# Optimization experiments

Hardware: AMD Instinct MI355X
Metric: run time of the kernel (lower is better)

The kernel has to match this reference:

```python
import jax, jax.numpy as jnp
import numpy as np

N, D, C = 4096, 2048, 8192
NUM_IDS = 256
MARGIN = 0.3
LABEL_SMOOTHING = 0.1


def setup_inputs() -> dict:
    key = jax.random.key(0)
    k1, k2, k3 = jax.random.split(key, 3)
    embeddings = jax.random.normal(k1, (N, D), dtype=jnp.float32)
    pred_ids = jax.random.normal(k2, (N, C), dtype=jnp.float32)
    target_ids = jax.random.randint(k3, (N,), 0, NUM_IDS, dtype=jnp.int64)
    return {"embeddings": embeddings, "pred_ids": pred_ids, "target_ids": target_ids}


def _euclidean_dist(x, y):
    xx = jnp.sum(x * x, axis=1, keepdims=True)            # [N,1]
    yy = jnp.sum(y * y, axis=1, keepdims=True).T          # [1,N]
    d2 = xx + yy - 2.0 * (x @ y.T)
    return jnp.sqrt(jnp.maximum(d2, 1e-12))


def _cross_entropy_ls(logits, targets, eps):
    # label-smoothed CE, mean over batch
    logp = jax.nn.log_softmax(logits, axis=-1)
    n_cls = logits.shape[-1]
    nll = -jnp.take_along_axis(logp, targets[:, None], axis=1)[:, 0]
    smooth = -jnp.mean(logp, axis=-1)
    return jnp.mean((1.0 - eps) * nll + eps * smooth)


def reference(embeddings, pred_ids, target_ids):
    # ID loss: cross entropy with label smoothing
    id_loss = _cross_entropy_ls(pred_ids, target_ids, LABEL_SMOOTHING)

    # Triplet loss with batch-hard mining
    dist = _euclidean_dist(embeddings, embeddings)        # [N,N]
    pos_mask = target_ids[:, None] == target_ids[None, :] # includes diagonal (as in original)
    neg_inf = jnp.float32(-jnp.inf)
    pos_inf = jnp.float32(jnp.inf)
    dist_ap = jnp.max(jnp.where(pos_mask, dist, neg_inf), axis=1)  # hardest positive
    dist_an = jnp.min(jnp.where(pos_mask, pos_inf, dist), axis=1)  # hardest negative

    # MarginRankingLoss with y=1: mean(relu(dist_ap - dist_an + margin))
    tri_loss = jnp.mean(jnp.maximum(dist_ap - dist_an + MARGIN, 0.0))

    return (id_loss, tri_loss, dist_ap, dist_an)
```

## Files before the change

### kernel.cpp

```cpp
#include <hip/hip_runtime.h>
#include <hip/hip_bf16.h>

typedef unsigned short u16;
typedef unsigned int u32;
typedef __attribute__((ext_vector_type(8))) __bf16 bf16x8;
typedef __attribute__((ext_vector_type(4))) float f32x4;

#define NROW 4096
#define DDIM 2048
#define NCLS 8192
#define MARGIN 0.3f
#define EPS_LS 0.1f
#define FLT_MAX_ 3.402823466e+38f

#define GLOBAL_AS __attribute__((address_space(1)))
#define LDS_AS __attribute__((address_space(3)))

__device__ __forceinline__ void gload_lds16(const void* g, void* l) {
    __builtin_amdgcn_global_load_lds((const GLOBAL_AS u32*)g, (LDS_AS u32*)l, 16, 0, 0);
}

__device__ __forceinline__ u16 f2bf(float f) {
    u32 b = __float_as_uint(f);
    u32 r = (b + 0x7FFFu + ((b >> 16) & 1u)) >> 16;
    return (u16)r;
}

__global__ __launch_bounds__(256) void prep_kernel(
    const float* __restrict__ emb, u16* __restrict__ e16,
    float* __restrict__ xx, int* __restrict__ ap, int* __restrict__ an)
{
    int row = blockIdx.x, tid = threadIdx.x;
    const float4* p = (const float4*)(emb + (size_t)row * DDIM);
    float4 a = p[tid * 2], b = p[tid * 2 + 1];
    float s = a.x*a.x + a.y*a.y + a.z*a.z + a.w*a.w
            + b.x*b.x + b.y*b.y + b.z*b.z + b.w*b.w;

    uint4 pk;
    pk.x = (u32)f2bf(a.x) | ((u32)f2bf(a.y) << 16);
    pk.y = (u32)f2bf(a.z) | ((u32)f2bf(a.w) << 16);
    pk.z = (u32)f2bf(b.x) | ((u32)f2bf(b.y) << 16);
    pk.w = (u32)f2bf(b.z) | ((u32)f2bf(b.w) << 16);
    *(uint4*)&e16[(size_t)row * DDIM + tid * 8] = pk;

    #pragma unroll
    for (int o = 1; o < 64; o <<= 1) s += __shfl_xor(s, o);
    __shared__ float sred[4];
    if ((tid & 63) == 0) sred[tid >> 6] = s;
    __syncthreads();
    if (tid == 0) {
        xx[row] = sred[0] + sred[1] + sred[2] + sred[3];
        ap[row] = 0x80000000;
        an[row] = 0x7FFFFFFF;
    }
}

__device__ __forceinline__ void ce_block(
    int row, const float* __restrict__ pred, const int* __restrict__ tgt,
    float* __restrict__ out, float* smem )
{
    int tid = threadIdx.x;
    const float4* p = (const float4*)(pred + (size_t)row * NCLS);
    float4 v[8];
    #pragma unroll
    for (int i = 0; i < 8; ++i) v[i] = p[tid + i * 256];

    float mx = -FLT_MAX_, sm = 0.f;
    #pragma unroll
    for (int i = 0; i < 8; ++i) {
        mx = fmaxf(mx, fmaxf(fmaxf(v[i].x, v[i].y), fmaxf(v[i].z, v[i].w)));
        sm += v[i].x + v[i].y + v[i].z + v[i].w;
    }
    #pragma unroll
    for (int o = 1; o < 64; o <<= 1) {
        mx = fmaxf(mx, __shfl_xor(mx, o));
        sm += __shfl_xor(sm, o);
    }
    float* smx = smem; float* ssm = smem + 4; float* sse = smem + 8;
    int w = tid >> 6;
    if ((tid & 63) == 0) { smx[w] = mx; ssm[w] = sm; }
    __syncthreads();
    mx = fmaxf(fmaxf(smx[0], smx[1]), fmaxf(smx[2], smx[3]));
    sm = ssm[0] + ssm[1] + ssm[2] + ssm[3];

    float es = 0.f;
    #pragma unroll
    for (int i = 0; i < 8; ++i) {
        es += expf(v[i].x - mx) + expf(v[i].y - mx)
            + expf(v[i].z - mx) + expf(v[i].w - mx);
    }
    #pragma unroll
    for (int o = 1; o < 64; o <<= 1) es += __shfl_xor(es, o);
    if ((tid & 63) == 0) sse[w] = es;
    __syncthreads();
    if (tid == 0) {
        es = sse[0] + sse[1] + sse[2] + sse[3];
        float lse = mx + logf(es);
        int t = tgt[row];
        float lt = pred[(size_t)row * NCLS + t];
        float loss = (1.0f - EPS_LS) * (lse - lt)
                   + EPS_LS * (lse - sm * (1.0f / NCLS));
        atomicAdd(out, loss * (1.0f / NROW));
    }
}

__global__ __launch_bounds__(256) void fused_kernel(
    const u16* __restrict__ e16, const float* __restrict__ xx,
    const int* __restrict__ tg, int* __restrict__ ap, int* __restrict__ an,
    const float* __restrict__ pred, float* __restrict__ out)
{
    __shared__ __align__(16) u16 lsA[64 * 64];
    __shared__ __align__(16) u16 lsB[128 * 64];
    __shared__ float cered[12];

    int bid = blockIdx.x;
    int q = bid / 5, rsel = bid - q * 5;
    if (rsel != 0) {
        int row = q * 4 + rsel - 1;
        if (row < NROW) ce_block(row, pred, tg, out, cered);
        return;
    }

    int g = q;
    int wg = ((g * 5) & 7) * 132 + (g >> 3);

    float sq = sqrtf(4225.0f - 4.0f * (float)wg);
    int m = (int)((65.0f - sq) * 0.5f);
    if (m < 0) m = 0;
    if (m > 31) m = 31;
    while (m > 0 && m * (65 - m) > wg) --m;
    while (m < 31 && (m + 1) * (64 - m) <= wg) ++m;
    int off = wg - m * (65 - m);
    int half = 32 - m;
    int r = 2 * m + (off >= half ? 1 : 0);
    int c = m + (off >= half ? off - half : off);
    int rowBase = r * 64, colBase = c * 128;

    int tid = threadIdx.x;
    int wid = tid >> 6, lane = tid & 63;
    int wm = wid >> 1, wn = wid & 1;

    f32x4 acc[2][4];
    #pragma unroll
    for (int i = 0; i < 2; ++i)
        #pragma unroll
        for (int j = 0; j < 4; ++j) acc[i][j] = (f32x4){0.f, 0.f, 0.f, 0.f};

    int srow = lane >> 3;
    int sslot = lane & 7;

    for (int kb = 0; kb < DDIM; kb += 64) {
        #pragma unroll
        for (int t = 0; t < 2; ++t) {
            int r0 = wid * 16 + t * 8;
            int rr = r0 + srow;
            int gsl = sslot ^ (rr & 7);
            gload_lds16(&e16[(size_t)(rowBase + rr) * DDIM + kb + gsl * 8],
                        &lsA[r0 * 64]);
        }
        #pragma unroll
        for (int t = 0; t < 4; ++t) {
            int r0 = wid * 32 + t * 8;
            int rr = r0 + srow;
            int gsl = sslot ^ (rr & 7);
            gload_lds16(&e16[(size_t)(colBase + rr) * DDIM + kb + gsl * 8],
                        &lsB[r0 * 64]);
        }
        __syncthreads();

        #pragma unroll
        for (int h = 0; h < 2; ++h) {
            bf16x8 af[2], bfr[4];
            #pragma unroll
            for (int fm = 0; fm < 2; ++fm) {
                int row = wm * 32 + fm * 16 + (lane & 15);
                int sl = (h * 4 + (lane >> 4)) ^ (row & 7);
                af[fm] = *(const bf16x8*)&lsA[row * 64 + sl * 8];
            }
            #pragma unroll
            for (int fn = 0; fn < 4; ++fn) {
                int row = wn * 64 + fn * 16 + (lane & 15);
                int sl = (h * 4 + (lane >> 4)) ^ (row & 7);
                bfr[fn] = *(const bf16x8*)&lsB[row * 64 + sl * 8];
            }
            #pragma unroll
            for (int fm = 0; fm < 2; ++fm)
                #pragma unroll
                for (int fn = 0; fn < 4; ++fn)
                    acc[fm][fn] = __builtin_amdgcn_mfma_f32_16x16x32_bf16(
                        af[fm], bfr[fn], acc[fm][fn], 0, 0, 0);
        }
        __syncthreads();
    }

    float xc[4]; int tc[4];
    float capc[4], canc[4];
    #pragma unroll
    for (int fn = 0; fn < 4; ++fn) {
        int gc = colBase + wn * 64 + fn * 16 + (lane & 15);
        xc[fn] = xx[gc];
        tc[fn] = tg[gc];
        capc[fn] = -FLT_MAX_;
        canc[fn] = FLT_MAX_;
    }
    #pragma unroll
    for (int fm = 0; fm < 2; ++fm) {
        #pragma unroll
        for (int reg = 0; reg < 4; ++reg) {
            int gr = rowBase + wm * 32 + fm * 16 + (lane >> 4) * 4 + reg;
            float xr = xx[gr];
            int   tr = tg[gr];
            float cap = -FLT_MAX_, can = FLT_MAX_;
            #pragma unroll
            for (int fn = 0; fn < 4; ++fn) {
                int gc = colBase + wn * 64 + fn * 16 + (lane & 15);
                float d2 = xr + xc[fn] - 2.0f * acc[fm][fn][reg];
                d2 = fmaxf(d2, 0.0f);
                if (gr == gc) d2 = 0.0f;
                bool pos = (tr == tc[fn]);
                if (pos) { cap = fmaxf(cap, d2); capc[fn] = fmaxf(capc[fn], d2); }
                else     { can = fminf(can, d2); canc[fn] = fminf(canc[fn], d2); }
            }
            #pragma unroll
            for (int o = 1; o < 16; o <<= 1) {
                cap = fmaxf(cap, __shfl_xor(cap, o));
                can = fminf(can, __shfl_xor(can, o));
            }
            if ((lane & 15) == 0) {
                atomicMax(&ap[gr], __float_as_int(cap));
                atomicMin(&an[gr], __float_as_int(can));
            }
        }
    }
    #pragma unroll
    for (int fn = 0; fn < 4; ++fn) {
        float cap = capc[fn], can = canc[fn];
        cap = fmaxf(cap, __shfl_xor(cap, 16));
        can = fminf(can, __shfl_xor(can, 16));
        cap = fmaxf(cap, __shfl_xor(cap, 32));
        can = fminf(can, __shfl_xor(can, 32));
        if (lane < 16) {
            int gc = colBase + wn * 64 + fn * 16 + lane;
            atomicMax(&ap[gc], __float_as_int(cap));
            atomicMin(&an[gc], __float_as_int(can));
        }
    }
}

__global__ __launch_bounds__(256) void final_kernel(
    const int* __restrict__ ap, const int* __restrict__ an,
    float* __restrict__ out)
{
    int i = blockIdx.x * 256 + threadIdx.x;
    float a2 = __int_as_float(ap[i]);
    float n2 = __int_as_float(an[i]);
    float av = sqrtf(fmaxf(a2, 1e-12f));
    float nv = sqrtf(fmaxf(n2, 1e-12f));
    out[2 + i] = av;
    out[2 + NROW + i] = nv;
    float t = fmaxf(av - nv + MARGIN, 0.0f);
    #pragma unroll
    for (int o = 1; o < 64; o <<= 1) t += __shfl_xor(t, o);
    __shared__ float sred[4];
    if ((threadIdx.x & 63) == 0) sred[threadIdx.x >> 6] = t;
    __syncthreads();
    if (threadIdx.x == 0)
        atomicAdd(out + 1, (sred[0] + sred[1] + sred[2] + sred[3]) * (1.0f / NROW));
}

extern "C" void kernel_launch(void* const* d_in, const int* in_sizes, int n_in,
                              void* d_out, int out_size, void* d_ws, size_t ws_size,
                              hipStream_t stream)
{
    const float* emb  = (const float*)d_in[0];
    const float* pred = (const float*)d_in[1];
    const int*   tgt  = (const int*)d_in[2];
    float* out = (float*)d_out;

    char* ws = (char*)d_ws;
    u16*   e16 = (u16*)ws;
    float* xx  = (float*)(ws + (size_t)16 * 1024 * 1024);
    int*   ap  = (int*)(ws + (size_t)16 * 1024 * 1024 + 16384);
    int*   an  = (int*)(ws + (size_t)16 * 1024 * 1024 + 32768);

    hipMemsetAsync(d_out, 0, 2 * sizeof(float), stream);
    prep_kernel <<<NROW, 256, 0, stream>>>(emb, e16, xx, ap, an);
    fused_kernel<<<5280, 256, 0, stream>>>(e16, xx, tgt, ap, an, pred, out);
    final_kernel<<<NROW / 256, 256, 0, stream>>>(ap, an, out);
}
```

Measured before the change: 294.7 us.

## Double-buffer LDS tiles to overlap global loads with MFMA compute

Splits the shared-memory A and B tiles into two buffers and prefetches the next K-slice with global_load_lds while MFMAs run on the current buffer. This halves the number of barriers per K step and aims to hide global-to-LDS latency in the Gram-matrix GEMM. It doubles LDS use per block, which may lower occupancy, and relies on the barrier that precedes each compute to make the async loads visible.

```diff
diff --git a/kernel.cpp b/kernel.cpp
--- a/kernel.cpp
+++ b/kernel.cpp
@@ -109,12 +109,14 @@
     const int* __restrict__ tg, int* __restrict__ ap, int* __restrict__ an,
     const float* __restrict__ pred, float* __restrict__ out)
 {
-    __shared__ __align__(16) u16 lsA[64 * 64];
-    __shared__ __align__(16) u16 lsB[128 * 64];
+    __shared__ __align__(16) u16 lsA[2][64 * 64];
+    __shared__ __align__(16) u16 lsB[2][128 * 64];
     __shared__ float cered[12];
 
     int bid = blockIdx.x;
+    int tid = threadIdx.x;
     int q = bid / 5, rsel = bid - q * 5;
+
     if (rsel != 0) {
         int row = q * 4 + rsel - 1;
         if (row < NROW) ce_block(row, pred, tg, out, cered);
@@ -136,7 +138,6 @@
     int c = m + (off >= half ? off - half : off);
     int rowBase = r * 64, colBase = c * 128;
 
-    int tid = threadIdx.x;
     int wid = tid >> 6, lane = tid & 63;
     int wm = wid >> 1, wn = wid & 1;
 
@@ -149,49 +150,64 @@
     int srow = lane >> 3;
     int sslot = lane & 7;
 
-    for (int kb = 0; kb < DDIM; kb += 64) {
-        #pragma unroll
-        for (int t = 0; t < 2; ++t) {
-            int r0 = wid * 16 + t * 8;
-            int rr = r0 + srow;
-            int gsl = sslot ^ (rr & 7);
-            gload_lds16(&e16[(size_t)(rowBase + rr) * DDIM + kb + gsl * 8],
-                        &lsA[r0 * 64]);
-        }
-        #pragma unroll
-        for (int t = 0; t < 4; ++t) {
-            int r0 = wid * 32 + t * 8;
-            int rr = r0 + srow;
-            int gsl = sslot ^ (rr & 7);
-            gload_lds16(&e16[(size_t)(colBase + rr) * DDIM + kb + gsl * 8],
-                        &lsB[r0 * 64]);
-        }
+#define STAGE(BUF, KB)                                                        \
+    {                                                                         \
+        _Pragma("unroll")                                                     \
+        for (int t = 0; t < 2; ++t) {                         \
+            int r0 = wid * 16 + t * 8;                                        \
+            int rr = r0 + srow;                                               \
+            int gsl = sslot ^ (rr & 7);                                       \
+            gload_lds16(&e16[(size_t)(rowBase + rr) * DDIM + (KB) + gsl * 8], \
+                        &lsA[BUF][r0 * 64]);                                  \
+        }                                                                     \
+        _Pragma("unroll")                                                     \
+        for (int t = 0; t < 4; ++t) {                        \
+            int r0 = wid * 32 + t * 8;                                        \
+            int rr = r0 + srow;                                               \
+            int gsl = sslot ^ (rr & 7);                                       \
+            gload_lds16(&e16[(size_t)(colBase + rr) * DDIM + (KB) + gsl * 8], \
+                        &lsB[BUF][r0 * 64]);                                  \
+        }                                                                     \
+    }
+
+#define COMPUTE(BUF)                                                          \
+    {                                                                         \
+        _Pragma("unroll")                                                     \
+        for (int h = 0; h < 2; ++h) {                                         \
+            bf16x8 af[2], bfr[4];                                             \
+            _Pragma("unroll")                                                 \
+            for (int fm = 0; fm < 2; ++fm) {                                  \
+                int row = wm * 32 + fm * 16 + (lane & 15);                    \
+                int sl = (h * 4 + (lane >> 4)) ^ (row & 7);                   \
+                af[fm] = *(const bf16x8*)&lsA[BUF][row * 64 + sl * 8];        \
+            }                                                                 \
+            _Pragma("unroll")                                                 \
+            for (int fn = 0; fn < 4; ++fn) {                                  \
+                int row = wn * 64 + fn * 16 + (lane & 15);                    \
+                int sl = (h * 4 + (lane >> 4)) ^ (row & 7);                   \
+                bfr[fn] = *(const bf16x8*)&lsB[BUF][row * 64 + sl * 8];       \
+            }                                                                 \
+            _Pragma("unroll")                                                 \
+            for (int fm = 0; fm < 2; ++fm)                                    \
+                _Pragma("unroll")                                             \
+                for (int fn = 0; fn < 4; ++fn)                                \
+                    acc[fm][fn] = __builtin_amdgcn_mfma_f32_16x16x32_bf16(    \
+                        af[fm], bfr[fn], acc[fm][fn], 0, 0, 0);               \
+        }                                                                     \
+    }
+
+    STAGE(0, 0);
+    __syncthreads();
+    for (int kb = 0; kb < DDIM; kb += 128) {
+        STAGE(1, kb + 64);
+        COMPUTE(0);
         __syncthreads();
-
-        #pragma unroll
-        for (int h = 0; h < 2; ++h) {
-            bf16x8 af[2], bfr[4];
-            #pragma unroll
-            for (int fm = 0; fm < 2; ++fm) {
-                int row = wm * 32 + fm * 16 + (lane & 15);
-                int sl = (h * 4 + (lane >> 4)) ^ (row & 7);
-                af[fm] = *(const bf16x8*)&lsA[row * 64 + sl * 8];
-            }
-            #pragma unroll
-            for (int fn = 0; fn < 4; ++fn) {
-                int row = wn * 64 + fn * 16 + (lane & 15);
-                int sl = (h * 4 + (lane >> 4)) ^ (row & 7);
-                bfr[fn] = *(const bf16x8*)&lsB[row * 64 + sl * 8];
-            }
-            #pragma unroll
-            for (int fm = 0; fm < 2; ++fm)
-                #pragma unroll
-                for (int fn = 0; fn < 4; ++fn)
-                    acc[fm][fn] = __builtin_amdgcn_mfma_f32_16x16x32_bf16(
-                        af[fm], bfr[fn], acc[fm][fn], 0, 0, 0);
-        }
+        if (kb + 128 < DDIM) STAGE(0, kb + 128);
+        COMPUTE(1);
         __syncthreads();
     }
+#undef STAGE
+#undef COMPUTE
 
     float xc[4]; int tc[4];
     float capc[4], canc[4];
```

Result: no change. 295.6 us (+0.3%).
